# Optimization experiments

Measured on AMD Instinct MI355X. Metric: run time of the kernel, lower is better.

## Reference

```python
import jax, jax.numpy as jnp
import numpy as np

B, T, QD, CD = 64, 1024, 1024, 512  # batch, encoder steps, query_dim, context_dim


def setup_inputs() -> dict:
    key = jax.random.key(0)
    k1, k2, k3, k4 = jax.random.split(key, 4)
    query = jax.random.normal(k1, (B, 1, QD), dtype=jnp.float32)
    inputs = jax.random.normal(k2, (B, T, CD), dtype=jnp.float32)
    # init_states: alpha = [1, 1e-7, 1e-7, ...], u = 0.5, sq = 1.4
    alpha = jnp.concatenate([jnp.ones((B, 1)), jnp.full((B, T - 1), 1e-7)], axis=1).astype(jnp.float32)
    u = jnp.full((B, 1), 0.5, dtype=jnp.float32)
    sq = jnp.full((B, 1), 1.4, dtype=jnp.float32)
    W_u = (jax.random.normal(k3, (QD + CD, 1)) * 0.02).astype(jnp.float32)
    b_u = jnp.zeros((1,), dtype=jnp.float32)
    W_sq = (jax.random.normal(k4, (QD + CD, 1)) * 0.02).astype(jnp.float32)
    b_sq = jnp.zeros((1,), dtype=jnp.float32)
    return {"query": query, "inputs": inputs, "alpha": alpha, "u": u, "sq": sq,
            "W_u": W_u, "b_u": b_u, "W_sq": W_sq, "b_sq": b_sq}


def reference(query, inputs, alpha, u, sq, W_u, b_u, W_sq, b_sq):
    # shift alpha forward by one step (pad a zero at position 0)
    fwd_shifted = jnp.pad(alpha[:, :-1], ((0, 0), (1, 0)))            # [B, T]
    a = ((1.0 - u) * alpha + u * fwd_shifted + 1e-6) ** sq           # [B, T]
    a = a / jnp.sum(a, axis=1, keepdims=True)                        # normalized alpha
    context = jnp.einsum('bt,btc->bc', a, inputs)                    # [B, CD]
    ta_input = jnp.concatenate([context, query[:, 0, :]], axis=-1)   # [B, CD+QD]
    u_new = jax.nn.sigmoid(ta_input @ W_u + b_u)                     # [B, 1]
    sq_new = jax.nn.sigmoid(ta_input @ W_sq + b_sq) + 1.0            # [B, 1] (dynamicsq)
    return context, a, u_new, sq_new
```

## Files before the change

kernel.cpp:

```cpp
#include <hip/hip_runtime.h>
#include <math.h>

#define B_  64
#define T_  1024
#define QD_ 1024
#define CD_ 512
#define SEGROWS_ 32
#define NBLK_ 16

typedef float floatx4 __attribute__((ext_vector_type(4)));

__global__ __launch_bounds__(256) void attn_ctx_all(
    const float* __restrict__ inputs, const float* __restrict__ alpha,
    const float* __restrict__ u, const float* __restrict__ sq,
    float* __restrict__ part, float* __restrict__ out_a)
{
    const int seg = blockIdx.x;
    const int b   = blockIdx.y;
    const int tid = threadIdx.x;

    __shared__ float s_alpha[T_];
    __shared__ float s_raw[T_];
    __shared__ float s_red[4];

    ((float4*)s_alpha)[tid] = ((const float4*)(alpha + (size_t)b * T_))[tid];
    __syncthreads();

    const float ub  = u[b];
    const float sqb = sq[b];
    const float omu = 1.0f - ub;

    float lsum = 0.f;
    float rr[4];
    const int t0 = tid * 4;
#pragma unroll
    for (int i = 0; i < 4; ++i) {
        const int t = t0 + i;
        const float prev = (t == 0) ? 0.f : s_alpha[t - 1];
        const float x = omu * s_alpha[t] + ub * prev + 1e-6f;
        const float r = __powf(x, sqb);
        rr[i] = r;
        lsum += r;
    }
    {
        float4 w; w.x = rr[0]; w.y = rr[1]; w.z = rr[2]; w.w = rr[3];
        ((float4*)s_raw)[tid] = w;
    }
#pragma unroll
    for (int off = 32; off > 0; off >>= 1) lsum += __shfl_down(lsum, off);
    if ((tid & 63) == 0) s_red[tid >> 6] = lsum;
    __syncthreads();
    const float inv = 1.0f / (s_red[0] + s_red[1] + s_red[2] + s_red[3]);

    const int lane  = tid & 127;
    const int half  = tid >> 7;
    const int tbase = seg * 64 + half * 32;

    const floatx4* in4 =
        (const floatx4*)(inputs + ((size_t)b * T_ + tbase) * CD_);
    float4 acc = {0.f, 0.f, 0.f, 0.f};
#pragma unroll 8
    for (int i = 0; i < 32; ++i) {
        const float av = s_raw[tbase + i];
        const floatx4 x = __builtin_nontemporal_load(&in4[(size_t)i * 128 + lane]);
        acc.x += av * x.x; acc.y += av * x.y; acc.z += av * x.z; acc.w += av * x.w;
    }
    acc.x *= inv; acc.y *= inv; acc.z *= inv; acc.w *= inv;

    const int prow = seg * 2 + half;
    ((float4*)(part + ((size_t)b * SEGROWS_ + prow) * CD_))[lane] = acc;

    if (seg == 0) {
        float4 o;
        o.x = rr[0] * inv; o.y = rr[1] * inv; o.z = rr[2] * inv; o.w = rr[3] * inv;
        ((float4*)(out_a + (size_t)b * T_))[tid] = o;
    }
}

__global__ __launch_bounds__(512) void attn_final(
    const float* __restrict__ part,
    const float* __restrict__ query,
    const float* __restrict__ W_u, const float* __restrict__ b_u,
    const float* __restrict__ W_sq, const float* __restrict__ b_sq,
    float* __restrict__ out_ctx, float* __restrict__ out_u,
    float* __restrict__ out_sq)
{
    const int b   = blockIdx.x;
    const int tid = threadIdx.x;

    float c = 0.f;
    const float* pb = part + (size_t)b * SEGROWS_ * CD_;
#pragma unroll 8
    for (int s = 0; s < SEGROWS_; ++s) c += pb[(size_t)s * CD_ + tid];
    out_ctx[(size_t)b * CD_ + tid] = c;

    const float* qb = query + (size_t)b * QD_;
    const float q0 = qb[tid];
    const float q1 = qb[tid + 512];

    float du = c * W_u[tid]  + q0 * W_u[512 + tid]  + q1 * W_u[1024 + tid];
    float ds = c * W_sq[tid] + q0 * W_sq[512 + tid] + q1 * W_sq[1024 + tid];
#pragma unroll
    for (int off = 32; off > 0; off >>= 1) {
        du += __shfl_down(du, off);
        ds += __shfl_down(ds, off);
    }
    __shared__ float s_u[8], s_s[8];
    if ((tid & 63) == 0) { s_u[tid >> 6] = du; s_s[tid >> 6] = ds; }
    __syncthreads();
    if (tid == 0) {
        float su = b_u[0], ss = b_sq[0];
#pragma unroll
        for (int w = 0; w < 8; ++w) { su += s_u[w]; ss += s_s[w]; }
        out_u[b]  = 1.0f / (1.0f + __expf(-su));
        out_sq[b] = 1.0f / (1.0f + __expf(-ss)) + 1.0f;
    }
}

__global__ __launch_bounds__(256) void attn_ctx_atomic(
    const float* __restrict__ inputs, const float* __restrict__ alpha,
    const float* __restrict__ u, const float* __restrict__ sq,
    float* __restrict__ ctx, float* __restrict__ out_a)
{
    const int seg = blockIdx.x;
    const int b   = blockIdx.y;
    const int tid = threadIdx.x;

    __shared__ float s_alpha[T_];
    __shared__ float s_raw[T_];
    __shared__ float s_red[4];

    ((float4*)s_alpha)[tid] = ((const float4*)(alpha + (size_t)b * T_))[tid];
    __syncthreads();

    const float ub  = u[b];
    const float sqb = sq[b];
    const float omu = 1.0f - ub;

    float lsum = 0.f;
    float rr[4];
    const int t0 = tid * 4;
#pragma unroll
    for (int i = 0; i < 4; ++i) {
        const int t = t0 + i;
        const float prev = (t == 0) ? 0.f : s_alpha[t - 1];
        const float x = omu * s_alpha[t] + ub * prev + 1e-6f;
        const float r = __powf(x, sqb);
        rr[i] = r; lsum += r;
    }
    {
        float4 w; w.x = rr[0]; w.y = rr[1]; w.z = rr[2]; w.w = rr[3];
        ((float4*)s_raw)[tid] = w;
    }
#pragma unroll
    for (int off = 32; off > 0; off >>= 1) lsum += __shfl_down(lsum, off);
    if ((tid & 63) == 0) s_red[tid >> 6] = lsum;
    __syncthreads();
    const float inv = 1.0f / (s_red[0] + s_red[1] + s_red[2] + s_red[3]);

    const int lane  = tid & 127;
    const int half  = tid >> 7;
    const int tbase = seg * 64 + half * 32;

    const float4* in4 =
        (const float4*)(inputs + ((size_t)b * T_ + tbase) * CD_);
    float4 acc = {0.f, 0.f, 0.f, 0.f};
    for (int i = 0; i < 32; ++i) {
        const float av = s_raw[tbase + i];
        const float4 x = in4[(size_t)i * 128 + lane];
        acc.x += av * x.x; acc.y += av * x.y; acc.z += av * x.z; acc.w += av * x.w;
    }
    float* dst = ctx + (size_t)b * CD_ + lane * 4;
    atomicAdd(dst + 0, acc.x * inv);
    atomicAdd(dst + 1, acc.y * inv);
    atomicAdd(dst + 2, acc.z * inv);
    atomicAdd(dst + 3, acc.w * inv);

    if (seg == 0) {
        float4 o;
        o.x = rr[0] * inv; o.y = rr[1] * inv; o.z = rr[2] * inv; o.w = rr[3] * inv;
        ((float4*)(out_a + (size_t)b * T_))[tid] = o;
    }
}

__global__ __launch_bounds__(512) void attn_heads(
    const float* __restrict__ query,
    const float* __restrict__ W_u, const float* __restrict__ b_u,
    const float* __restrict__ W_sq, const float* __restrict__ b_sq,
    const float* __restrict__ out_ctx, float* __restrict__ out_u,
    float* __restrict__ out_sq)
{
    const int b   = blockIdx.x;
    const int tid = threadIdx.x;

    const float c  = out_ctx[(size_t)b * CD_ + tid];
    const float* qb = query + (size_t)b * QD_;
    const float q0 = qb[tid];
    const float q1 = qb[tid + 512];

    float du = c * W_u[tid]  + q0 * W_u[512 + tid]  + q1 * W_u[1024 + tid];
    float ds = c * W_sq[tid] + q0 * W_sq[512 + tid] + q1 * W_sq[1024 + tid];
#pragma unroll
    for (int off = 32; off > 0; off >>= 1) {
        du += __shfl_down(du, off);
        ds += __shfl_down(ds, off);
    }
    __shared__ float s_u[8], s_s[8];
    if ((tid & 63) == 0) { s_u[tid >> 6] = du; s_s[tid >> 6] = ds; }
    __syncthreads();
    if (tid == 0) {
        float su = b_u[0], ss = b_sq[0];
#pragma unroll
        for (int w = 0; w < 8; ++w) { su += s_u[w]; ss += s_s[w]; }
        out_u[b]  = 1.0f / (1.0f + __expf(-su));
        out_sq[b] = 1.0f / (1.0f + __expf(-ss)) + 1.0f;
    }
}

extern "C" void kernel_launch(void* const* d_in, const int* in_sizes, int n_in,
                              void* d_out, int out_size, void* d_ws, size_t ws_size,
                              hipStream_t stream) {
    const float* query  = (const float*)d_in[0];
    const float* inputs = (const float*)d_in[1];
    const float* alpha  = (const float*)d_in[2];
    const float* u      = (const float*)d_in[3];
    const float* sq     = (const float*)d_in[4];
    const float* W_u    = (const float*)d_in[5];
    const float* b_u    = (const float*)d_in[6];
    const float* W_sq   = (const float*)d_in[7];
    const float* b_sq   = (const float*)d_in[8];

    float* out      = (float*)d_out;
    float* out_ctx  = out;
    float* out_a    = out + (size_t)B_ * CD_;
    float* out_u    = out_a + (size_t)B_ * T_;
    float* out_sq   = out_u + B_;

    const size_t part_bytes = (size_t)B_ * SEGROWS_ * CD_ * sizeof(float);

    if (ws_size >= part_bytes) {
        float* part = (float*)d_ws;
        attn_ctx_all<<<dim3(NBLK_, B_), 256, 0, stream>>>(
            inputs, alpha, u, sq, part, out_a);
        attn_final<<<B_, 512, 0, stream>>>(
            part, query, W_u, b_u, W_sq, b_sq, out_ctx, out_u, out_sq);
    } else {
        (void)hipMemsetAsync(out_ctx, 0, (size_t)B_ * CD_ * sizeof(float), stream);
        attn_ctx_atomic<<<dim3(NBLK_, B_), 256, 0, stream>>>(
            inputs, alpha, u, sq, out_ctx, out_a);
        attn_heads<<<B_, 512, 0, stream>>>(
            query, W_u, b_u, W_sq, b_sq, out_ctx, out_u, out_sq);
    }
}
```

Baseline: 201.6 us.

## Prefetch input rows before alpha normalization and combine halves in shared memory

The context kernel now issues the first eight nontemporal input loads before computing the alpha power and block-sum reduction, then keeps an 8-deep register ring of prefetched rows in a fully unrolled loop. The intent is to overlap global-memory latency with the alpha math. It also drops the shared alpha/raw arrays: alpha is read straight from global memory and only the block's own 64 weights are kept in shared memory. The two half-block partial sums are merged through shared memory, which halves the partial buffer rows the final kernel must read, at the cost of an extra barrier and more register pressure.

```diff
diff --git a/kernel.cpp b/kernel.cpp
--- a/kernel.cpp
+++ b/kernel.cpp
@@ -5,7 +5,7 @@
 #define T_  1024
 #define QD_ 1024
 #define CD_ 512
-#define SEGROWS_ 32
+#define SEGROWS_ 16
 #define NBLK_ 16
 
 typedef float floatx4 __attribute__((ext_vector_type(4)));
@@ -19,61 +19,79 @@
     const int b   = blockIdx.y;
     const int tid = threadIdx.x;
 
-    __shared__ float s_alpha[T_];
-    __shared__ float s_raw[T_];
-    __shared__ float s_red[4];
-
-    ((float4*)s_alpha)[tid] = ((const float4*)(alpha + (size_t)b * T_))[tid];
-    __syncthreads();
-
-    const float ub  = u[b];
-    const float sqb = sq[b];
-    const float omu = 1.0f - ub;
-
-    float lsum = 0.f;
-    float rr[4];
-    const int t0 = tid * 4;
-#pragma unroll
-    for (int i = 0; i < 4; ++i) {
-        const int t = t0 + i;
-        const float prev = (t == 0) ? 0.f : s_alpha[t - 1];
-        const float x = omu * s_alpha[t] + ub * prev + 1e-6f;
-        const float r = __powf(x, sqb);
-        rr[i] = r;
-        lsum += r;
-    }
-    {
-        float4 w; w.x = rr[0]; w.y = rr[1]; w.z = rr[2]; w.w = rr[3];
-        ((float4*)s_raw)[tid] = w;
-    }
-#pragma unroll
-    for (int off = 32; off > 0; off >>= 1) lsum += __shfl_down(lsum, off);
-    if ((tid & 63) == 0) s_red[tid >> 6] = lsum;
-    __syncthreads();
-    const float inv = 1.0f / (s_red[0] + s_red[1] + s_red[2] + s_red[3]);
+    __shared__ float  s_seg[64];
+    __shared__ float  s_red[4];
+    __shared__ float4 s_comb[128];
 
     const int lane  = tid & 127;
     const int half  = tid >> 7;
     const int tbase = seg * 64 + half * 32;
-
     const floatx4* in4 =
         (const floatx4*)(inputs + ((size_t)b * T_ + tbase) * CD_);
+
+    const int t0 = tid * 4;
+    const float4 a4   = ((const float4*)(alpha + (size_t)b * T_))[tid];
+    const float aprev = (tid == 0) ? 0.f : alpha[(size_t)b * T_ + t0 - 1];
+    const float ub    = u[b];
+    const float sqb   = sq[b];
+
+    floatx4 xf[8];
+#pragma unroll
+    for (int i = 0; i < 8; ++i)
+        xf[i] = __builtin_nontemporal_load(&in4[(size_t)i * 128 + lane]);
+
+    const float omu = 1.0f - ub;
+    float rr[4];
+    float lsum;
+    {
+        const float x0 = omu * a4.x + ub * aprev + 1e-6f;
+        const float x1 = omu * a4.y + ub * a4.x  + 1e-6f;
+        const float x2 = omu * a4.z + ub * a4.y  + 1e-6f;
+        const float x3 = omu * a4.w + ub * a4.z  + 1e-6f;
+        rr[0] = __powf(x0, sqb);
+        rr[1] = __powf(x1, sqb);
+        rr[2] = __powf(x2, sqb);
+        rr[3] = __powf(x3, sqb);
+        lsum = (rr[0] + rr[1]) + (rr[2] + rr[3]);
+    }
+
+    if ((tid >> 4) == seg) {
+        const int o = t0 - seg * 64;
+        s_seg[o + 0] = rr[0]; s_seg[o + 1] = rr[1];
+        s_seg[o + 2] = rr[2]; s_seg[o + 3] = rr[3];
+    }
+
+#pragma unroll
+    for (int off = 32; off > 0; off >>= 1) lsum += __shfl_down(lsum, off);
+    if ((tid & 63) == 0) s_red[tid >> 6] = lsum;
+    __syncthreads();
+    const float inv = 1.0f / (s_red[0] + s_red[1] + s_red[2] + s_red[3]);
+
     float4 acc = {0.f, 0.f, 0.f, 0.f};
-#pragma unroll 8
+#pragma unroll
     for (int i = 0; i < 32; ++i) {
-        const float av = s_raw[tbase + i];
-        const floatx4 x = __builtin_nontemporal_load(&in4[(size_t)i * 128 + lane]);
-        acc.x += av * x.x; acc.y += av * x.y; acc.z += av * x.z; acc.w += av * x.w;
-    }
-    acc.x *= inv; acc.y *= inv; acc.z *= inv; acc.w *= inv;
-
-    const int prow = seg * 2 + half;
-    ((float4*)(part + ((size_t)b * SEGROWS_ + prow) * CD_))[lane] = acc;
+        const floatx4 x = xf[i & 7];
+        if (i + 8 < 32)
+            xf[i & 7] = __builtin_nontemporal_load(&in4[(size_t)(i + 8) * 128 + lane]);
+        const float av = s_seg[half * 32 + i];
+        acc.x += av * x.x; acc.y += av * x.y;
+        acc.z += av * x.z; acc.w += av * x.w;
+    }
 
     if (seg == 0) {
         float4 o;
         o.x = rr[0] * inv; o.y = rr[1] * inv; o.z = rr[2] * inv; o.w = rr[3] * inv;
         ((float4*)(out_a + (size_t)b * T_))[tid] = o;
+    }
+
+    if (half == 1) s_comb[lane] = acc;
+    __syncthreads();
+    if (half == 0) {
+        const float4 o2 = s_comb[lane];
+        float4 w;
+        w.x = (acc.x + o2.x) * inv; w.y = (acc.y + o2.y) * inv;
+        w.z = (acc.z + o2.z) * inv; w.w = (acc.w + o2.w) * inv;
+        ((float4*)(part + ((size_t)b * SEGROWS_ + seg) * CD_))[lane] = w;
     }
 }
 
@@ -90,7 +108,7 @@
 
     float c = 0.f;
     const float* pb = part + (size_t)b * SEGROWS_ * CD_;
-#pragma unroll 8
+#pragma unroll
     for (int s = 0; s < SEGROWS_; ++s) c += pb[(size_t)s * CD_ + tid];
     out_ctx[(size_t)b * CD_ + tid] = c;
 
```

New measurement: 199.6 us. Within noise of the previous version (-1.0%).
